# Kernel tuning notes

Measured on AMD Instinct MI355X. Metric: run time of the kernel, lower is better.

## Reference

```python
import jax, jax.numpy as jnp
import numpy as np

T, B, OBS, H, P, L, A = 512, 128, 512, 256, 128, 4, 4


def _ln(x, scale, bias, eps=1e-6):
    mu = jnp.mean(x, axis=-1, keepdims=True)
    var = jnp.mean((x - mu) ** 2, axis=-1, keepdims=True)
    return (x - mu) * jax.lax.rsqrt(var + eps) * scale + bias


def _binop(qi, qj):
    # S5 reset-aware associative operator: elements (A, b, reset_flag)
    Ai, bi, ci = qi
    Aj, bj, cj = qj
    A = (Aj * Ai) * (1.0 - cj) + Aj * cj
    b = (Aj * bi + bj) * (1.0 - cj) + bj * cj
    c = ci * (1.0 - cj) + cj
    return A, b, c


def _s5_layer(x, dones, h0, scale, bias, lam_re, lam_im, b_re, b_im, c_re, c_im, d_vec, log_step, glu_W, glu_b):
    # x: (T,B,H) real, dones: (T,B), h0: (B,P) complex64
    skip = x
    u = _ln(x, scale, bias)                                  # prenorm
    lam = lam_re + 1j * lam_im                               # (P,)
    step = jnp.exp(log_step)                                 # (P,)
    lam_bar = jnp.exp(lam * step)                            # ZOH discretization
    B_bar = ((lam_bar - 1.0) / lam)[:, None] * (b_re + 1j * b_im)  # (P,H)
    Bu = jnp.einsum('tbh,ph->tbp', u.astype(jnp.complex64), B_bar)  # (T,B,P)
    A_el = jnp.concatenate([jnp.ones((1, B, P), jnp.complex64),
                            jnp.broadcast_to(lam_bar.astype(jnp.complex64), (T, B, P))], axis=0)
    b_el = jnp.concatenate([h0[None], Bu], axis=0)
    c_el = jnp.concatenate([jnp.zeros((1, B, 1), jnp.float32), dones[..., None]], axis=0)
    _, xs, _ = jax.lax.associative_scan(_binop, (A_el, b_el, c_el), axis=0)
    xs = xs[1:]                                              # (T,B,P) complex states
    new_h = xs[-1]
    C = c_re + 1j * c_im                                     # (H,P)
    ys = 2.0 * jnp.real(jnp.einsum('tbp,hp->tbh', xs, C)) + d_vec * u  # conj_sym output + D*u
    z = _ln(ys, scale, bias)                                 # gtrxl norm (shared LayerNorm params)
    z = jax.nn.gelu(z)                                       # half_glu1
    z = z * jax.nn.sigmoid(z @ glu_W + glu_b)
    return skip + z, new_h


def setup_inputs() -> dict:
    key = jax.random.key(0)
    ks = jax.random.split(key, 40)
    f32 = jnp.float32

    def n(i, shape, s=1.0):
        return jax.random.normal(ks[i], shape, f32) * s

    inp = {}
    inp['obs'] = n(0, (T, B, OBS))
    inp['dones'] = (jax.random.uniform(ks[1], (T, B)) < 0.01).astype(f32)
    inp['hidden_re'] = jnp.zeros((L, B, P), f32)
    inp['hidden_im'] = jnp.zeros((L, B, P), f32)
    inp['enc0_W'] = n(2, (OBS, 128), 1.0 / np.sqrt(OBS))
    inp['enc0_b'] = jnp.zeros((128,), f32)
    inp['enc1_W'] = n(3, (128, H), 1.0 / np.sqrt(128))
    inp['enc1_b'] = jnp.zeros((H,), f32)
    inp['norm_scale'] = jnp.ones((L, H), f32)
    inp['norm_bias'] = jnp.zeros((L, H), f32)
    inp['Lambda_re'] = -0.5 * jax.random.uniform(ks[4], (L, P), f32) - 0.1
    inp['Lambda_im'] = n(5, (L, P), np.pi)
    inp['B_re'] = n(6, (L, P, H), 1.0 / np.sqrt(H))
    inp['B_im'] = n(7, (L, P, H), 1.0 / np.sqrt(H))
    inp['C_re'] = n(8, (L, H, P), 1.0 / np.sqrt(2 * P))
    inp['C_im'] = n(9, (L, H, P), 1.0 / np.sqrt(2 * P))
    inp['D'] = n(10, (L, H))
    inp['log_step'] = jax.random.uniform(ks[11], (L, P), f32, np.log(1e-3), np.log(1e-1))
    inp['glu_W'] = n(12, (L, H, H), 1.0 / np.sqrt(H))
    inp['glu_b'] = jnp.zeros((L, H), f32)
    inp['ab0_W'] = n(13, (H, 128), 1.0 / np.sqrt(H))
    inp['ab0_b'] = jnp.zeros((128,), f32)
    inp['ab1_W'] = n(14, (128, 128), 1.0 / np.sqrt(128))
    inp['ab1_b'] = jnp.zeros((128,), f32)
    inp['adec_W'] = n(15, (128, A), 0.01 / np.sqrt(128))
    inp['adec_b'] = jnp.full((A,), 0.5, f32)
    inp['log_std'] = jnp.full((A,), -0.7, f32)
    inp['vb0_W'] = n(16, (H, 128), 1.0 / np.sqrt(H))
    inp['vb0_b'] = jnp.zeros((128,), f32)
    inp['vb1_W'] = n(17, (128, 128), 1.0 / np.sqrt(128))
    inp['vb1_b'] = jnp.zeros((128,), f32)
    inp['vdec_W'] = n(18, (128, 1), 1.0 / np.sqrt(128))
    inp['vdec_b'] = jnp.zeros((1,), f32)
    return inp


def reference(obs, dones, hidden_re, hidden_im, enc0_W, enc0_b, enc1_W, enc1_b,
              norm_scale, norm_bias, Lambda_re, Lambda_im, B_re, B_im, C_re, C_im,
              D, log_step, glu_W, glu_b, ab0_W, ab0_b, ab1_W, ab1_b, adec_W, adec_b,
              log_std, vb0_W, vb0_b, vb1_W, vb1_b, vdec_W, vdec_b):
    e = jax.nn.leaky_relu(obs @ enc0_W + enc0_b)
    e = jax.nn.leaky_relu(e @ enc1_W + enc1_b)
    h0 = (hidden_re + 1j * hidden_im).astype(jnp.complex64)  # (L,B,P)
    new_h = []
    for l in range(L):
        e, hl = _s5_layer(e, dones, h0[l], norm_scale[l], norm_bias[l],
                          Lambda_re[l], Lambda_im[l], B_re[l], B_im[l],
                          C_re[l], C_im[l], D[l], log_step[l], glu_W[l], glu_b[l])
        new_h.append(hl)
    new_h = jnp.stack(new_h)
    am = jax.nn.leaky_relu(e @ ab0_W + ab0_b)
    am = jax.nn.leaky_relu(am @ ab1_W + ab1_b)
    am = am @ adec_W + adec_b                                # actor mean (T,B,A)
    v = jax.nn.leaky_relu(e @ vb0_W + vb0_b)
    v = jax.nn.leaky_relu(v @ vb1_W + vb1_b)
    v = v @ vdec_W + vdec_b                                  # critic (T,B,1)
    sc = jnp.broadcast_to(jnp.exp(log_std), am.shape)        # Normal scale (pi params)
    out = jnp.concatenate([am, sc, v], axis=-1)              # (T,B,2A+1)
    return out, jnp.real(new_h), jnp.imag(new_h)
```

## Files before the change

kernel.cpp:

```cpp
#include <hip/hip_runtime.h>
#include <math.h>

#define TT 512
#define BB 128
#define OBSD 512
#define HD 256
#define PD 128
#define LD 4
#define NTB (TT*BB)

typedef __bf16 bf16x8 __attribute__((ext_vector_type(8)));
typedef float  f32x4  __attribute__((ext_vector_type(4)));

__device__ __forceinline__ float bf2f(unsigned short u) {
    return __uint_as_float(((unsigned)u) << 16);
}
__device__ __forceinline__ unsigned short f2bf(float f) {
    unsigned u = __float_as_uint(f);
    unsigned r = (u + 0x7FFFu + ((u >> 16) & 1u)) >> 16;
    return (unsigned short)r;
}
__device__ __forceinline__ float gelu_f(float x) {
    float x3 = x * x * x;
    return 0.5f * x * (1.f + tanhf(0.7978845608028654f * (x + 0.044715f * x3)));
}

__device__ __forceinline__ void stage_tile4(const unsigned short* gbase, int ldk,
                                            int row0, int k0, unsigned short* sm, int tid)
{
    int w = tid >> 6, lane = tid & 63;
#pragma unroll
    for (int p = 0; p < 2; ++p) {
        int r = p * 64 + w * 16 + (lane >> 2);
        const unsigned short* g = gbase + (size_t)(row0 + r) * ldk + k0 + (lane & 3) * 8;
        unsigned short* l = sm + (p * 64 + w * 16) * 32;
        __builtin_amdgcn_global_load_lds(
            (const __attribute__((address_space(1))) void*)g,
            (__attribute__((address_space(3))) void*)l, 16, 0, 0);
    }
}

__device__ __forceinline__ void stage_tile8(const unsigned short* gbase, int ldk,
                                            int row0, int k0, unsigned short* sm, int tid)
{
    int w = tid >> 6, lane = tid & 63;
    int r = w * 16 + (lane >> 2);
    const unsigned short* g = gbase + (size_t)(row0 + r) * ldk + k0 + (lane & 3) * 8;
    unsigned short* l = sm + w * 16 * 32;
    __builtin_amdgcn_global_load_lds(
        (const __attribute__((address_space(1))) void*)g,
        (__attribute__((address_space(3))) void*)l, 16, 0, 0);
}
__device__ __forceinline__ void stage_tile8w(const unsigned short* gbase, int ldk,
                                             int row0, int k0, unsigned short* sm, int tid)
{
    int w = tid >> 6, lane = tid & 63;
#pragma unroll
    for (int p = 0; p < 2; ++p) {
        int r = p * 128 + w * 16 + (lane >> 2);
        const unsigned short* g = gbase + (size_t)(row0 + r) * ldk + k0 + (lane & 3) * 8;
        unsigned short* l = sm + (p * 128 + w * 16) * 32;
        __builtin_amdgcn_global_load_lds(
            (const __attribute__((address_space(1))) void*)g,
            (__attribute__((address_space(3))) void*)l, 16, 0, 0);
    }
}

template<int MODE>
__global__ __launch_bounds__(512) void mgemm2(
    const unsigned short* __restrict__ A, const unsigned short* __restrict__ BT,
    int K, const float* __restrict__ bias,
    const float* __restrict__ lnsc, const float* __restrict__ lnbi,
    const unsigned short* __restrict__ aux1, unsigned short* Xio,
    unsigned short* __restrict__ U, int wU)
{
    __shared__ unsigned short smA[128 * 32];
    __shared__ unsigned short smB[256 * 32];
    __shared__ float2 red[128][4];
    int tid = threadIdx.x;
    int lane = tid & 63, w = tid >> 6;
    int wr = w & 1, wc = w >> 1;
    int m16 = lane & 15, quad = lane >> 4;
    int m0 = blockIdx.x * 128;

    f32x4 acc[4][4] = {};

    for (int k0 = 0; k0 < K; k0 += 32) {
        stage_tile8(A, K, m0, k0, smA, tid);
        stage_tile8w(BT, K, 0, k0, smB, tid);
        __syncthreads();
        bf16x8 af[4], bfr[4];
#pragma unroll
        for (int mi = 0; mi < 4; ++mi)
            af[mi] = *(const bf16x8*)(smA + (wr * 64 + mi * 16 + m16) * 32 + quad * 8);
#pragma unroll
        for (int nj = 0; nj < 4; ++nj)
            bfr[nj] = *(const bf16x8*)(smB + (wc * 64 + nj * 16 + m16) * 32 + quad * 8);
#pragma unroll
        for (int mi = 0; mi < 4; ++mi)
#pragma unroll
            for (int nj = 0; nj < 4; ++nj)
                acc[mi][nj] = __builtin_amdgcn_mfma_f32_16x16x32_bf16(
                    af[mi], bfr[nj], acc[mi][nj], 0, 0, 0);
        __syncthreads();
    }

    int colb = wc * 64 + m16;
    if (MODE == 1) {
#pragma unroll
        for (int mi = 0; mi < 4; ++mi)
#pragma unroll
            for (int nj = 0; nj < 4; ++nj)
#pragma unroll
                for (int r = 0; r < 4; ++r) {
                    int row = m0 + wr * 64 + mi * 16 + quad * 4 + r;
                    U[(size_t)row * 256 + colb + nj * 16] = f2bf(acc[mi][nj][r]);
                }
        return;
    }

    float bn[4];
#pragma unroll
    for (int nj = 0; nj < 4; ++nj) bn[nj] = bias[colb + nj * 16];

#pragma unroll
    for (int mi = 0; mi < 4; ++mi) {
#pragma unroll
        for (int r = 0; r < 4; ++r) {
            int row_l = wr * 64 + mi * 16 + quad * 4 + r;
            size_t rowb = (size_t)(m0 + row_l) * 256;
            float s = 0.f, q = 0.f;
#pragma unroll
            for (int nj = 0; nj < 4; ++nj) {
                size_t idx = rowb + colb + nj * 16;
                float v = acc[mi][nj][r];
                if (MODE == 0) {
                    v += bn[nj]; v = v > 0.f ? v : 0.01f * v;
                    Xio[idx] = f2bf(v);
                } else if (MODE == 2) {
                    v += bn[nj] * bf2f(aux1[idx]);
                } else if (MODE == 3) {
                    float sg = 1.f / (1.f + expf(-(v + bn[nj])));
                    v = bf2f(Xio[idx]) + bf2f(aux1[idx]) * sg;
                    Xio[idx] = f2bf(v);
                }
                acc[mi][nj][r] = v;
                s += v; q += v * v;
            }
            if (MODE != 3 || wU) {
#pragma unroll
                for (int mask = 1; mask < 16; mask <<= 1) {
                    s += __shfl_xor(s, mask);
                    q += __shfl_xor(q, mask);
                }
                if (m16 == 0) red[row_l][wc] = float2{s, q};
            }
        }
    }
    if (MODE == 3 && !wU) return;
    __syncthreads();

    float ls[4], lb[4];
#pragma unroll
    for (int nj = 0; nj < 4; ++nj) { ls[nj] = lnsc[colb + nj * 16]; lb[nj] = lnbi[colb + nj * 16]; }
#pragma unroll
    for (int mi = 0; mi < 4; ++mi) {
#pragma unroll
        for (int r = 0; r < 4; ++r) {
            int row_l = wr * 64 + mi * 16 + quad * 4 + r;
            float2 t0 = red[row_l][0], t1 = red[row_l][1], t2 = red[row_l][2], t3 = red[row_l][3];
            float S = t0.x + t1.x + t2.x + t3.x;
            float Q = t0.y + t1.y + t2.y + t3.y;
            float mu = S * (1.f / 256.f);
            float var = Q * (1.f / 256.f) - mu * mu;
            float rstd = rsqrtf(var + 1e-6f);
            size_t rowb = (size_t)(m0 + row_l) * 256;
#pragma unroll
            for (int nj = 0; nj < 4; ++nj) {
                float o = (acc[mi][nj][r] - mu) * rstd * ls[nj] + lb[nj];
                if (MODE == 2) o = gelu_f(o);
                U[rowb + colb + nj * 16] = f2bf(o);
            }
        }
    }
}

__global__ __launch_bounds__(256) void mgemm(
    const unsigned short* __restrict__ A, const unsigned short* __restrict__ BT,
    unsigned short* __restrict__ C, int M, int N, int K,
    const float* __restrict__ bias)
{
    __shared__ unsigned short smA[128 * 32];
    __shared__ unsigned short smB[128 * 32];
    int tid = threadIdx.x;
    int lane = tid & 63, w = tid >> 6;
    int wr = w & 1, wc = w >> 1;
    int m16 = lane & 15, quad = lane >> 4;
    int m0 = blockIdx.x * 128, n0 = blockIdx.y * 128;

    f32x4 acc[4][4] = {};
    for (int k0 = 0; k0 < K; k0 += 32) {
        stage_tile4(A, K, m0, k0, smA, tid);
        stage_tile4(BT, K, n0, k0, smB, tid);
        __syncthreads();
        bf16x8 af[4], bfr[4];
#pragma unroll
        for (int mi = 0; mi < 4; ++mi)
            af[mi] = *(const bf16x8*)(smA + (wr * 64 + mi * 16 + m16) * 32 + quad * 8);
#pragma unroll
        for (int nj = 0; nj < 4; ++nj)
            bfr[nj] = *(const bf16x8*)(smB + (wc * 64 + nj * 16 + m16) * 32 + quad * 8);
#pragma unroll
        for (int mi = 0; mi < 4; ++mi)
#pragma unroll
            for (int nj = 0; nj < 4; ++nj)
                acc[mi][nj] = __builtin_amdgcn_mfma_f32_16x16x32_bf16(
                    af[mi], bfr[nj], acc[mi][nj], 0, 0, 0);
        __syncthreads();
    }
#pragma unroll
    for (int mi = 0; mi < 4; ++mi)
#pragma unroll
        for (int nj = 0; nj < 4; ++nj) {
            int mg = m0 + wr * 64 + mi * 16 + quad * 4;
            int ng = n0 + wc * 64 + nj * 16 + m16;
            float bv = bias[ng];
#pragma unroll
            for (int r = 0; r < 4; ++r) {
                float v = acc[mi][nj][r] + bv;
                v = v > 0.f ? v : 0.01f * v;
                C[(size_t)(mg + r) * N + ng] = f2bf(v);
            }
        }
}

__global__ __launch_bounds__(512) void scan2_k(
    const unsigned short* __restrict__ bu, unsigned short* __restrict__ xs,
    const float* __restrict__ dones,
    const float* __restrict__ h0re, const float* __restrict__ h0im,
    const float* __restrict__ lamre, const float* __restrict__ lamim,
    const float* __restrict__ lstep,
    float* __restrict__ outre, float* __restrict__ outim)
{
    __shared__ float sdone[TT];
    __shared__ float4 ssum[8][64];
    __shared__ float2 shin[8][64];
    int tid = threadIdx.x;
    int b  = blockIdx.x >> 1;
    int ph = blockIdx.x & 1;
    int chunk = tid >> 6, pl = tid & 63;
    int p = ph * 64 + pl;
    sdone[tid] = dones[tid * BB + b];
    float lr = lamre[p], li = lamim[p];
    float st = expf(lstep[p]);
    float er = expf(lr * st);
    float ar = er * cosf(li * st);
    float ai = er * sinf(li * st);
    __syncthreads();

    int t0 = chunk * 64;
    unsigned buf[64];
    float Ar = 1.f, Ai = 0.f, br = 0.f, bi = 0.f;
#pragma unroll
    for (int j = 0; j < 64; ++j) {
        size_t base = ((size_t)(t0 + j) * BB + b) * 256;
        unsigned short rr = bu[base + p];
        unsigned short ii = bu[base + 128 + p];
        buf[j] = ((unsigned)ii << 16) | rr;
        float bur = bf2f(rr), bui = bf2f(ii);
        if (sdone[t0 + j] != 0.f) {
            Ar = 0.f; Ai = 0.f; br = bur; bi = bui;
        } else {
            float nAr = ar * Ar - ai * Ai;
            float nAi = ar * Ai + ai * Ar;
            float nbr = fmaf(ar, br, fmaf(-ai, bi, bur));
            float nbi = fmaf(ar, bi, fmaf(ai, br, bui));
            Ar = nAr; Ai = nAi; br = nbr; bi = nbi;
        }
    }
    ssum[chunk][pl] = float4{Ar, Ai, br, bi};
    __syncthreads();
    if (tid < 64) {
        int gid = b * 128 + p;
        float hr = h0re[gid], hi = h0im[gid];
#pragma unroll
        for (int c = 0; c < 8; ++c) {
            shin[c][pl] = float2{hr, hi};
            float4 s = ssum[c][pl];
            float nhr = fmaf(s.x, hr, fmaf(-s.y, hi, s.z));
            float nhi = fmaf(s.x, hi, fmaf(s.y, hr, s.w));
            hr = nhr; hi = nhi;
        }
        outre[gid] = hr; outim[gid] = hi;
    }
    __syncthreads();
    float hr = shin[chunk][pl].x, hi = shin[chunk][pl].y;
#pragma unroll
    for (int j = 0; j < 64; ++j) {
        unsigned v = buf[j];
        float bur = bf2f((unsigned short)(v & 0xFFFFu));
        float bui = bf2f((unsigned short)(v >> 16));
        float nr, ni;
        if (sdone[t0 + j] != 0.f) { nr = bur; ni = bui; }
        else {
            nr = fmaf(ar, hr, fmaf(-ai, hi, bur));
            ni = fmaf(ar, hi, fmaf(ai, hr, bui));
        }
        hr = nr; hi = ni;
        size_t base = ((size_t)(t0 + j) * BB + b) * 256;
        xs[base + p] = f2bf(nr);
        xs[base + 128 + p] = f2bf(ni);
    }
}

__global__ __launch_bounds__(256) void prep_k(
    const float* __restrict__ Br, const float* __restrict__ Bi,
    const float* __restrict__ Cr, const float* __restrict__ Ci,
    const float* __restrict__ Lr, const float* __restrict__ Li,
    const float* __restrict__ ls, unsigned short* bbarT, unsigned short* ccatT)
{
    int gid = blockIdx.x * 256 + threadIdx.x;
    int l = gid >> 15;
    int rem = gid & 32767;
    int p = rem >> 8;
    int h = rem & 255;
    float lr = Lr[l * PD + p], li = Li[l * PD + p];
    float st = expf(ls[l * PD + p]);
    float er = expf(lr * st);
    float lbr = er * cosf(li * st);
    float lbi = er * sinf(li * st);
    float nr = lbr - 1.f, ni = lbi;
    float den = lr * lr + li * li;
    float fr = (nr * lr + ni * li) / den;
    float fi = (ni * lr - nr * li) / den;
    float bre = Br[(size_t)(l * PD + p) * HD + h];
    float bim = Bi[(size_t)(l * PD + p) * HD + h];
    size_t lb = (size_t)l * 65536;
    bbarT[lb + (size_t)p * 256 + h]         = f2bf(fr * bre - fi * bim);
    bbarT[lb + (size_t)(128 + p) * 256 + h] = f2bf(fr * bim + fi * bre);
    float cre = Cr[(size_t)(l * HD + h) * PD + p];
    float cim = Ci[(size_t)(l * HD + h) * PD + p];
    ccatT[lb + (size_t)h * 256 + p]         = f2bf(2.f * cre);
    ccatT[lb + (size_t)h * 256 + 128 + p]   = f2bf(-2.f * cim);
}

__global__ __launch_bounds__(256) void tcvt_k(const float* __restrict__ in,
    unsigned short* __restrict__ out, int K, int N)
{
    int gid = blockIdx.x * 256 + threadIdx.x;
    if (gid >= K * N) return;
    int k = gid / N, n = gid - k * N;
    out[(size_t)n * K + k] = f2bf(in[gid]);
}

__global__ __launch_bounds__(256) void cvt_k(const float* __restrict__ in,
    unsigned short* __restrict__ out)
{
    size_t gid = (size_t)blockIdx.x * 256 + threadIdx.x;
    float4 v = ((const float4*)in)[gid];
    ushort4 o = { f2bf(v.x), f2bf(v.y), f2bf(v.z), f2bf(v.w) };
    ((ushort4*)out)[gid] = o;
}

__global__ __launch_bounds__(256) void head_k(
    const unsigned short* __restrict__ am2, const unsigned short* __restrict__ v2,
    const float* __restrict__ adW, const float* __restrict__ adb,
    const float* __restrict__ lstd,
    const float* __restrict__ vdW, const float* __restrict__ vdb,
    float* out)
{
    int wid = threadIdx.x >> 6, lane = threadIdx.x & 63;
    size_t row = (size_t)blockIdx.x * 4 + wid;
    float a1 = bf2f(am2[row * 128 + lane]);
    float a2 = bf2f(am2[row * 128 + 64 + lane]);
    float w1 = bf2f(v2[row * 128 + lane]);
    float w2 = bf2f(v2[row * 128 + 64 + lane]);
    float vals[5];
#pragma unroll
    for (int a = 0; a < 4; ++a)
        vals[a] = a1 * adW[lane * 4 + a] + a2 * adW[(lane + 64) * 4 + a];
    vals[4] = w1 * vdW[lane] + w2 * vdW[64 + lane];
#pragma unroll
    for (int off = 32; off; off >>= 1)
#pragma unroll
        for (int k = 0; k < 5; ++k) vals[k] += __shfl_xor(vals[k], off);
    if (lane == 0) {
        size_t o = row * 9;
#pragma unroll
        for (int a = 0; a < 4; ++a) out[o + a] = vals[a] + adb[a];
#pragma unroll
        for (int a = 0; a < 4; ++a) out[o + 4 + a] = expf(lstd[a]);
        out[o + 8] = vals[4] + vdb[0];
    }
}

extern "C" void kernel_launch(void* const* d_in, const int* in_sizes, int n_in,
                              void* d_out, int out_size, void* d_ws, size_t ws_size,
                              hipStream_t stream) {
    (void)in_sizes; (void)n_in; (void)out_size; (void)ws_size;
    const float* obs     = (const float*)d_in[0];
    const float* dones   = (const float*)d_in[1];
    const float* hre     = (const float*)d_in[2];
    const float* him     = (const float*)d_in[3];
    const float* enc0_W  = (const float*)d_in[4];
    const float* enc0_b  = (const float*)d_in[5];
    const float* enc1_W  = (const float*)d_in[6];
    const float* enc1_b  = (const float*)d_in[7];
    const float* nsc     = (const float*)d_in[8];
    const float* nbi     = (const float*)d_in[9];
    const float* Lre     = (const float*)d_in[10];
    const float* Lim     = (const float*)d_in[11];
    const float* B_re    = (const float*)d_in[12];
    const float* B_im    = (const float*)d_in[13];
    const float* C_re    = (const float*)d_in[14];
    const float* C_im    = (const float*)d_in[15];
    const float* Dv      = (const float*)d_in[16];
    const float* lstep   = (const float*)d_in[17];
    const float* glu_W   = (const float*)d_in[18];
    const float* glu_b   = (const float*)d_in[19];
    const float* ab0_W   = (const float*)d_in[20];
    const float* ab0_b   = (const float*)d_in[21];
    const float* ab1_W   = (const float*)d_in[22];
    const float* ab1_b   = (const float*)d_in[23];
    const float* adec_W  = (const float*)d_in[24];
    const float* adec_b  = (const float*)d_in[25];
    const float* log_std = (const float*)d_in[26];
    const float* vb0_W   = (const float*)d_in[27];
    const float* vb0_b   = (const float*)d_in[28];
    const float* vb1_W   = (const float*)d_in[29];
    const float* vb1_b   = (const float*)d_in[30];
    const float* vdec_W  = (const float*)d_in[31];
    const float* vdec_b  = (const float*)d_in[32];

    const size_t MB = (size_t)1 << 20;
    char* wsb = (char*)d_ws;
    unsigned short* OBSBF = (unsigned short*)(wsb);
    unsigned short* XS    = (unsigned short*)(wsb);
    unsigned short* AM1   = (unsigned short*)(wsb);
    unsigned short* V1    = (unsigned short*)(wsb + 16 * MB);
    unsigned short* AM2   = (unsigned short*)(wsb + 32 * MB);
    unsigned short* V2    = (unsigned short*)(wsb + 48 * MB);
    unsigned short* U1    = (unsigned short*)(wsb + 64 * MB);
    unsigned short* X     = (unsigned short*)(wsb + 96 * MB);
    unsigned short* U     = (unsigned short*)(wsb + 128 * MB);
    unsigned short* BU    = (unsigned short*)(wsb + 160 * MB);
    char* wgt = wsb + 192 * MB;
    unsigned short* BBART = (unsigned short*)(wgt);
    unsigned short* CCATT = (unsigned short*)(wgt + 512 * 1024);
    unsigned short* GLUT  = (unsigned short*)(wgt + 1024 * 1024);
    unsigned short* E0T   = (unsigned short*)(wgt + 1536 * 1024);
    unsigned short* E1T   = (unsigned short*)(wgt + 1664 * 1024);
    unsigned short* AB0T  = (unsigned short*)(wgt + 1728 * 1024);
    unsigned short* AB1T  = (unsigned short*)(wgt + 1792 * 1024);
    unsigned short* VB0T  = (unsigned short*)(wgt + 1824 * 1024);
    unsigned short* VB1T  = (unsigned short*)(wgt + 1888 * 1024);

    float* out   = (float*)d_out;
    float* outre = out + (size_t)NTB * 9;
    float* outim = outre + LD * BB * PD;

    prep_k<<<512, 256, 0, stream>>>(B_re, B_im, C_re, C_im, Lre, Lim, lstep, BBART, CCATT);
    tcvt_k<<<256, 256, 0, stream>>>(enc0_W, E0T, 512, 128);
    tcvt_k<<<128, 256, 0, stream>>>(enc1_W, E1T, 128, 256);
    for (int l = 0; l < LD; ++l)
        tcvt_k<<<256, 256, 0, stream>>>(glu_W + (size_t)l * 65536, GLUT + (size_t)l * 65536, 256, 256);
    tcvt_k<<<128, 256, 0, stream>>>(ab0_W, AB0T, 256, 128);
    tcvt_k<<<64, 256, 0, stream>>>(ab1_W, AB1T, 128, 128);
    tcvt_k<<<128, 256, 0, stream>>>(vb0_W, VB0T, 256, 128);
    tcvt_k<<<64, 256, 0, stream>>>(vb1_W, VB1T, 128, 128);
    cvt_k<<<32768, 256, 0, stream>>>(obs, OBSBF);

    mgemm<<<dim3(512, 1), 256, 0, stream>>>(OBSBF, E0T, U1, NTB, 128, 512, enc0_b);
    mgemm2<0><<<512, 512, 0, stream>>>(U1, E1T, 128, enc1_b, nsc, nbi, nullptr, X, U, 1);

    for (int l = 0; l < LD; ++l) {
        mgemm2<1><<<512, 512, 0, stream>>>(U, BBART + (size_t)l * 65536, 256,
                                           nullptr, nullptr, nullptr, nullptr, nullptr, BU, 0);
        scan2_k<<<256, 512, 0, stream>>>(BU, XS, dones, hre + l * BB * PD, him + l * BB * PD,
                                         Lre + l * PD, Lim + l * PD, lstep + l * PD,
                                         outre + l * BB * PD, outim + l * BB * PD);
        mgemm2<2><<<512, 512, 0, stream>>>(XS, CCATT + (size_t)l * 65536, 256,
                                           Dv + l * HD, nsc + l * HD, nbi + l * HD, U, nullptr, U, 1);
        const float* nsc2 = nsc + ((l + 1 < LD) ? (l + 1) * HD : 0);
        const float* nbi2 = nbi + ((l + 1 < LD) ? (l + 1) * HD : 0);
        mgemm2<3><<<512, 512, 0, stream>>>(U, GLUT + (size_t)l * 65536, 256,
                                           glu_b + l * HD, nsc2, nbi2, U, X, U, (l + 1 < LD) ? 1 : 0);
    }

    mgemm<<<dim3(512, 1), 256, 0, stream>>>(X, AB0T, AM1, NTB, 128, 256, ab0_b);
    mgemm<<<dim3(512, 1), 256, 0, stream>>>(AM1, AB1T, AM2, NTB, 128, 128, ab1_b);
    mgemm<<<dim3(512, 1), 256, 0, stream>>>(X, VB0T, V1, NTB, 128, 256, vb0_b);
    mgemm<<<dim3(512, 1), 256, 0, stream>>>(V1, VB1T, V2, NTB, 128, 128, vb1_b);
    head_k<<<NTB / 4, 256, 0, stream>>>(AM2, V2, adec_W, adec_b, log_std, vdec_W, vdec_b, out);
}
```

Measured before the change: 1.004 ms.

## Fuse obs bf16 conversion into encoder GEMM and interleave complex layout

Removes the separate fp32-to-bf16 conversion pass over the observation tensor by converting inside a new encoder GEMM kernel that reads fp32 directly, so the bf16 copy is never written to or read back from memory. It also changes the complex state layout from split real/imag halves to interleaved pairs, so the scan does one 32-bit load and one 32-bit store per element instead of two 16-bit accesses. The B-bar and C weight layouts are permuted to match, keeping the GEMM contractions the same. The fused GEMM reloads fp32 A tiles without double buffering, which may stall its main loop.

Result: slower. 1.199 ms (+19.5%).

```diff
diff --git a/kernel.cpp b/kernel.cpp
--- a/kernel.cpp
+++ b/kernel.cpp
@@ -234,6 +234,62 @@
         }
 }
 
+__global__ __launch_bounds__(256) void mgemm_obs(
+    const float* __restrict__ A, const unsigned short* __restrict__ BT,
+    unsigned short* __restrict__ C, int M, int N, int K,
+    const float* __restrict__ bias)
+{
+    __shared__ unsigned short smA[128 * 32];
+    __shared__ unsigned short smB[128 * 32];
+    int tid = threadIdx.x;
+    int lane = tid & 63, w = tid >> 6;
+    int wr = w & 1, wc = w >> 1;
+    int m16 = lane & 15, quad = lane >> 4;
+    int m0 = blockIdx.x * 128, n0 = blockIdx.y * 128;
+
+    f32x4 acc[4][4] = {};
+    for (int k0 = 0; k0 < K; k0 += 32) {
+#pragma unroll
+        for (int it = 0; it < 4; ++it) {
+            int idx = it * 256 + tid;
+            int r = idx >> 3, kq = (idx & 7) * 4;
+            float4 v = *(const float4*)(A + (size_t)(m0 + r) * K + k0 + kq);
+            ushort4 o = { f2bf(v.x), f2bf(v.y), f2bf(v.z), f2bf(v.w) };
+            *(ushort4*)(smA + r * 32 + kq) = o;
+        }
+        stage_tile4(BT, K, n0, k0, smB, tid);
+        __syncthreads();
+        bf16x8 af[4], bfr[4];
+#pragma unroll
+        for (int mi = 0; mi < 4; ++mi)
+            af[mi] = *(const bf16x8*)(smA + (wr * 64 + mi * 16 + m16) * 32 + quad * 8);
+#pragma unroll
+        for (int nj = 0; nj < 4; ++nj)
+            bfr[nj] = *(const bf16x8*)(smB + (wc * 64 + nj * 16 + m16) * 32 + quad * 8);
+#pragma unroll
+        for (int mi = 0; mi < 4; ++mi)
+#pragma unroll
+            for (int nj = 0; nj < 4; ++nj)
+                acc[mi][nj] = __builtin_amdgcn_mfma_f32_16x16x32_bf16(
+                    af[mi], bfr[nj], acc[mi][nj], 0, 0, 0);
+        __syncthreads();
+    }
+#pragma unroll
+    for (int mi = 0; mi < 4; ++mi)
+#pragma unroll
+        for (int nj = 0; nj < 4; ++nj) {
+            int mg = m0 + wr * 64 + mi * 16 + quad * 4;
+            int ng = n0 + wc * 64 + nj * 16 + m16;
+            float bv = bias[ng];
+#pragma unroll
+            for (int r = 0; r < 4; ++r) {
+                float v = acc[mi][nj][r] + bv;
+                v = v > 0.f ? v : 0.01f * v;
+                C[(size_t)(mg + r) * N + ng] = f2bf(v);
+            }
+        }
+}
+
 __global__ __launch_bounds__(512) void scan2_k(
     const unsigned short* __restrict__ bu, unsigned short* __restrict__ xs,
     const float* __restrict__ dones,
@@ -263,11 +319,11 @@
     float Ar = 1.f, Ai = 0.f, br = 0.f, bi = 0.f;
 #pragma unroll
     for (int j = 0; j < 64; ++j) {
-        size_t base = ((size_t)(t0 + j) * BB + b) * 256;
-        unsigned short rr = bu[base + p];
-        unsigned short ii = bu[base + 128 + p];
-        buf[j] = ((unsigned)ii << 16) | rr;
-        float bur = bf2f(rr), bui = bf2f(ii);
+        size_t off = ((size_t)(t0 + j) * BB + b) * 256 + 2 * p;
+        unsigned v = *(const unsigned*)(bu + off);
+        buf[j] = v;
+        float bur = bf2f((unsigned short)(v & 0xFFFFu));
+        float bui = bf2f((unsigned short)(v >> 16));
         if (sdone[t0 + j] != 0.f) {
             Ar = 0.f; Ai = 0.f; br = bur; bi = bui;
         } else {
@@ -307,9 +363,8 @@
             ni = fmaf(ar, hi, fmaf(ai, hr, bui));
         }
         hr = nr; hi = ni;
-        size_t base = ((size_t)(t0 + j) * BB + b) * 256;
-        xs[base + p] = f2bf(nr);
-        xs[base + 128 + p] = f2bf(ni);
+        size_t off = ((size_t)(t0 + j) * BB + b) * 256 + 2 * p;
+        *(unsigned*)(xs + off) = ((unsigned)f2bf(ni) << 16) | f2bf(nr);
     }
 }
 
@@ -336,12 +391,12 @@
     float bre = Br[(size_t)(l * PD + p) * HD + h];
     float bim = Bi[(size_t)(l * PD + p) * HD + h];
     size_t lb = (size_t)l * 65536;
-    bbarT[lb + (size_t)p * 256 + h]         = f2bf(fr * bre - fi * bim);
-    bbarT[lb + (size_t)(128 + p) * 256 + h] = f2bf(fr * bim + fi * bre);
+    bbarT[lb + (size_t)(2 * p) * 256 + h]     = f2bf(fr * bre - fi * bim);
+    bbarT[lb + (size_t)(2 * p + 1) * 256 + h] = f2bf(fr * bim + fi * bre);
     float cre = Cr[(size_t)(l * HD + h) * PD + p];
     float cim = Ci[(size_t)(l * HD + h) * PD + p];
-    ccatT[lb + (size_t)h * 256 + p]         = f2bf(2.f * cre);
-    ccatT[lb + (size_t)h * 256 + 128 + p]   = f2bf(-2.f * cim);
+    ccatT[lb + (size_t)h * 256 + 2 * p]     = f2bf(2.f * cre);
+    ccatT[lb + (size_t)h * 256 + 2 * p + 1] = f2bf(-2.f * cim);
 }
 
 __global__ __launch_bounds__(256) void tcvt_k(const float* __restrict__ in,
@@ -351,15 +406,6 @@
     if (gid >= K * N) return;
     int k = gid / N, n = gid - k * N;
     out[(size_t)n * K + k] = f2bf(in[gid]);
-}
-
-__global__ __launch_bounds__(256) void cvt_k(const float* __restrict__ in,
-    unsigned short* __restrict__ out)
-{
-    size_t gid = (size_t)blockIdx.x * 256 + threadIdx.x;
-    float4 v = ((const float4*)in)[gid];
-    ushort4 o = { f2bf(v.x), f2bf(v.y), f2bf(v.z), f2bf(v.w) };
-    ((ushort4*)out)[gid] = o;
 }
 
 __global__ __launch_bounds__(256) void head_k(
@@ -434,7 +480,6 @@
 
     const size_t MB = (size_t)1 << 20;
     char* wsb = (char*)d_ws;
-    unsigned short* OBSBF = (unsigned short*)(wsb);
     unsigned short* XS    = (unsigned short*)(wsb);
     unsigned short* AM1   = (unsigned short*)(wsb);
     unsigned short* V1    = (unsigned short*)(wsb + 16 * MB);
@@ -468,9 +513,8 @@
     tcvt_k<<<64, 256, 0, stream>>>(ab1_W, AB1T, 128, 128);
     tcvt_k<<<128, 256, 0, stream>>>(vb0_W, VB0T, 256, 128);
     tcvt_k<<<64, 256, 0, stream>>>(vb1_W, VB1T, 128, 128);
-    cvt_k<<<32768, 256, 0, stream>>>(obs, OBSBF);
-
-    mgemm<<<dim3(512, 1), 256, 0, stream>>>(OBSBF, E0T, U1, NTB, 128, 512, enc0_b);
+
+    mgemm_obs<<<dim3(512, 1), 256, 0, stream>>>(obs, E0T, U1, NTB, 128, 512, enc0_b);
     mgemm2<0><<<512, 512, 0, stream>>>(U1, E1T, 128, enc1_b, nsc, nbi, nullptr, X, U, 1);
 
     for (int l = 0; l < LD; ++l) {
```

## Restructure GEMMs to 64-row tiles with transposed MFMA, fuse obs conversion, interleave complex layout

Applied to the files above, without the earlier changes.

All GEMMs now use 64-row tiles with 256-thread blocks and swap the MFMA operands, so each lane holds four consecutive columns and can write or read them as one ushort4. The obs fp32-to-bf16 conversion is folded into the first encoder GEMM's staging, which removes a separate pass over the input. Real and imaginary parts in the Bbar/C weights and in the BU/XS buffers are interleaved so the scan does single 32-bit loads and stores. The trade-off is smaller tiles, which give less operand reuse per block, and register-path staging for obs instead of direct-to-LDS loads.

Measured after the change: 984.7 us. About the same (-1.9%).

```diff
diff --git a/kernel.cpp b/kernel.cpp
--- a/kernel.cpp
+++ b/kernel.cpp
@@ -25,213 +25,218 @@
     return 0.5f * x * (1.f + tanhf(0.7978845608028654f * (x + 0.044715f * x3)));
 }
 
-__device__ __forceinline__ void stage_tile4(const unsigned short* gbase, int ldk,
-                                            int row0, int k0, unsigned short* sm, int tid)
-{
-    int w = tid >> 6, lane = tid & 63;
-#pragma unroll
-    for (int p = 0; p < 2; ++p) {
-        int r = p * 64 + w * 16 + (lane >> 2);
-        const unsigned short* g = gbase + (size_t)(row0 + r) * ldk + k0 + (lane & 3) * 8;
-        unsigned short* l = sm + (p * 64 + w * 16) * 32;
-        __builtin_amdgcn_global_load_lds(
-            (const __attribute__((address_space(1))) void*)g,
-            (__attribute__((address_space(3))) void*)l, 16, 0, 0);
-    }
-}
-
-__device__ __forceinline__ void stage_tile8(const unsigned short* gbase, int ldk,
-                                            int row0, int k0, unsigned short* sm, int tid)
-{
-    int w = tid >> 6, lane = tid & 63;
-    int r = w * 16 + (lane >> 2);
-    const unsigned short* g = gbase + (size_t)(row0 + r) * ldk + k0 + (lane & 3) * 8;
-    unsigned short* l = sm + w * 16 * 32;
-    __builtin_amdgcn_global_load_lds(
-        (const __attribute__((address_space(1))) void*)g,
-        (__attribute__((address_space(3))) void*)l, 16, 0, 0);
-}
-__device__ __forceinline__ void stage_tile8w(const unsigned short* gbase, int ldk,
-                                             int row0, int k0, unsigned short* sm, int tid)
-{
-    int w = tid >> 6, lane = tid & 63;
-#pragma unroll
-    for (int p = 0; p < 2; ++p) {
-        int r = p * 128 + w * 16 + (lane >> 2);
-        const unsigned short* g = gbase + (size_t)(row0 + r) * ldk + k0 + (lane & 3) * 8;
-        unsigned short* l = sm + (p * 128 + w * 16) * 32;
-        __builtin_amdgcn_global_load_lds(
-            (const __attribute__((address_space(1))) void*)g,
-            (__attribute__((address_space(3))) void*)l, 16, 0, 0);
-    }
-}
-
-template<int MODE>
-__global__ __launch_bounds__(512) void mgemm2(
+template<int MODE, int NJ>
+__global__ __launch_bounds__(256) void mgemm2(
     const unsigned short* __restrict__ A, const unsigned short* __restrict__ BT,
     int K, const float* __restrict__ bias,
     const float* __restrict__ lnsc, const float* __restrict__ lnbi,
     const unsigned short* __restrict__ aux1, unsigned short* Xio,
     unsigned short* __restrict__ U, int wU)
 {
-    __shared__ unsigned short smA[128 * 32];
-    __shared__ unsigned short smB[256 * 32];
-    __shared__ float2 red[128][4];
+    const int N = NJ * 64;
+    __shared__ unsigned short smA[64 * 32];
+    __shared__ unsigned short smB[NJ * 64 * 32];
+    __shared__ float2 red[64][4];
     int tid = threadIdx.x;
     int lane = tid & 63, w = tid >> 6;
-    int wr = w & 1, wc = w >> 1;
     int m16 = lane & 15, quad = lane >> 4;
-    int m0 = blockIdx.x * 128;
-
-    f32x4 acc[4][4] = {};
+    int m0 = blockIdx.x * 64;
+
+    f32x4 acc[4][NJ] = {};
 
     for (int k0 = 0; k0 < K; k0 += 32) {
-        stage_tile8(A, K, m0, k0, smA, tid);
-        stage_tile8w(BT, K, 0, k0, smB, tid);
+        {
+            const unsigned short* g = A + (size_t)(m0 + (tid >> 2)) * K + k0 + (tid & 3) * 8;
+            unsigned short* l = smA + tid * 8;
+            __builtin_amdgcn_global_load_lds(
+                (const __attribute__((address_space(1))) void*)g,
+                (__attribute__((address_space(3))) void*)l, 16, 0, 0);
+        }
+#pragma unroll
+        for (int p = 0; p < NJ; ++p) {
+            const unsigned short* g = BT + (size_t)(p * 64 + (tid >> 2)) * K + k0 + (tid & 3) * 8;
+            unsigned short* l = smB + p * 2048 + tid * 8;
+            __builtin_amdgcn_global_load_lds(
+                (const __attribute__((address_space(1))) void*)g,
+                (__attribute__((address_space(3))) void*)l, 16, 0, 0);
+        }
         __syncthreads();
-        bf16x8 af[4], bfr[4];
+        bf16x8 af[4], bfr[NJ];
 #pragma unroll
         for (int mi = 0; mi < 4; ++mi)
-            af[mi] = *(const bf16x8*)(smA + (wr * 64 + mi * 16 + m16) * 32 + quad * 8);
-#pragma unroll
-        for (int nj = 0; nj < 4; ++nj)
-            bfr[nj] = *(const bf16x8*)(smB + (wc * 64 + nj * 16 + m16) * 32 + quad * 8);
+            af[mi] = *(const bf16x8*)(smA + (mi * 16 + m16) * 32 + quad * 8);
+#pragma unroll
+        for (int nj = 0; nj < NJ; ++nj)
+            bfr[nj] = *(const bf16x8*)(smB + (w * NJ * 16 + nj * 16 + m16) * 32 + quad * 8);
 #pragma unroll
         for (int mi = 0; mi < 4; ++mi)
 #pragma unroll
-            for (int nj = 0; nj < 4; ++nj)
+            for (int nj = 0; nj < NJ; ++nj)
                 acc[mi][nj] = __builtin_amdgcn_mfma_f32_16x16x32_bf16(
-                    af[mi], bfr[nj], acc[mi][nj], 0, 0, 0);
+                    bfr[nj], af[mi], acc[mi][nj], 0, 0, 0);
         __syncthreads();
     }
 
-    int colb = wc * 64 + m16;
+    int colb = w * NJ * 16 + quad * 4;
+
     if (MODE == 1) {
 #pragma unroll
-        for (int mi = 0; mi < 4; ++mi)
-#pragma unroll
-            for (int nj = 0; nj < 4; ++nj)
-#pragma unroll
-                for (int r = 0; r < 4; ++r) {
-                    int row = m0 + wr * 64 + mi * 16 + quad * 4 + r;
-                    U[(size_t)row * 256 + colb + nj * 16] = f2bf(acc[mi][nj][r]);
+        for (int mi = 0; mi < 4; ++mi) {
+            size_t rowb = (size_t)(m0 + mi * 16 + m16) * N;
+#pragma unroll
+            for (int nj = 0; nj < NJ; ++nj) {
+                ushort4 o = { f2bf(acc[mi][nj][0]), f2bf(acc[mi][nj][1]),
+                              f2bf(acc[mi][nj][2]), f2bf(acc[mi][nj][3]) };
+                *(ushort4*)(U + rowb + colb + nj * 16) = o;
+            }
+        }
+        return;
+    }
+
+    float4 bn[NJ];
+#pragma unroll
+    for (int nj = 0; nj < NJ; ++nj) bn[nj] = *(const float4*)(bias + colb + nj * 16);
+
+#pragma unroll
+    for (int mi = 0; mi < 4; ++mi) {
+        size_t rowb = (size_t)(m0 + mi * 16 + m16) * N;
+        float s = 0.f, q = 0.f;
+#pragma unroll
+        for (int nj = 0; nj < NJ; ++nj) {
+            ushort4 a1, xo;
+            if (MODE == 2 || MODE == 3) a1 = *(const ushort4*)(aux1 + rowb + colb + nj * 16);
+            if (MODE == 3)              xo = *(const ushort4*)(Xio + rowb + colb + nj * 16);
+            float vv[4];
+#pragma unroll
+            for (int r = 0; r < 4; ++r) {
+                float v = acc[mi][nj][r];
+                float bv = (r == 0) ? bn[nj].x : (r == 1) ? bn[nj].y : (r == 2) ? bn[nj].z : bn[nj].w;
+                if (MODE == 0 || MODE == 4) {
+                    v += bv; v = v > 0.f ? v : 0.01f * v;
+                } else if (MODE == 2) {
+                    float u = bf2f(r == 0 ? a1.x : r == 1 ? a1.y : r == 2 ? a1.z : a1.w);
+                    v += bv * u;
+                } else if (MODE == 3) {
+                    float zz = bf2f(r == 0 ? a1.x : r == 1 ? a1.y : r == 2 ? a1.z : a1.w);
+                    float xx = bf2f(r == 0 ? xo.x : r == 1 ? xo.y : r == 2 ? xo.z : xo.w);
+                    float sg = 1.f / (1.f + expf(-(v + bv)));
+                    v = xx + zz * sg;
                 }
-        return;
-    }
-
-    float bn[4];
-#pragma unroll
-    for (int nj = 0; nj < 4; ++nj) bn[nj] = bias[colb + nj * 16];
-
-#pragma unroll
-    for (int mi = 0; mi < 4; ++mi) {
-#pragma unroll
-        for (int r = 0; r < 4; ++r) {
-            int row_l = wr * 64 + mi * 16 + quad * 4 + r;
-            size_t rowb = (size_t)(m0 + row_l) * 256;
-            float s = 0.f, q = 0.f;
-#pragma unroll
-            for (int nj = 0; nj < 4; ++nj) {
-                size_t idx = rowb + colb + nj * 16;
-                float v = acc[mi][nj][r];
-                if (MODE == 0) {
-                    v += bn[nj]; v = v > 0.f ? v : 0.01f * v;
-                    Xio[idx] = f2bf(v);
-                } else if (MODE == 2) {
-                    v += bn[nj] * bf2f(aux1[idx]);
-                } else if (MODE == 3) {
-                    float sg = 1.f / (1.f + expf(-(v + bn[nj])));
-                    v = bf2f(Xio[idx]) + bf2f(aux1[idx]) * sg;
-                    Xio[idx] = f2bf(v);
-                }
+                vv[r] = v;
                 acc[mi][nj][r] = v;
                 s += v; q += v * v;
             }
-            if (MODE != 3 || wU) {
-#pragma unroll
-                for (int mask = 1; mask < 16; mask <<= 1) {
-                    s += __shfl_xor(s, mask);
-                    q += __shfl_xor(q, mask);
-                }
-                if (m16 == 0) red[row_l][wc] = float2{s, q};
+            if (MODE == 0 || MODE == 3) {
+                ushort4 o = { f2bf(vv[0]), f2bf(vv[1]), f2bf(vv[2]), f2bf(vv[3]) };
+                *(ushort4*)(Xio + rowb + colb + nj * 16) = o;
+            } else if (MODE == 4) {
+                ushort4 o = { f2bf(vv[0]), f2bf(vv[1]), f2bf(vv[2]), f2bf(vv[3]) };
+                *(ushort4*)(U + rowb + colb + nj * 16) = o;
             }
         }
-    }
-    if (MODE == 3 && !wU) return;
+        if (MODE != 4 && (MODE != 3 || wU)) {
+            s += __shfl_xor(s, 16); q += __shfl_xor(q, 16);
+            s += __shfl_xor(s, 32); q += __shfl_xor(q, 32);
+            if (quad == 0) red[mi * 16 + m16][w] = float2{s, q};
+        }
+    }
+    if (MODE == 4 || (MODE == 3 && !wU)) return;
     __syncthreads();
 
-    float ls[4], lb[4];
-#pragma unroll
-    for (int nj = 0; nj < 4; ++nj) { ls[nj] = lnsc[colb + nj * 16]; lb[nj] = lnbi[colb + nj * 16]; }
+    float4 ls[NJ], lb[NJ];
+#pragma unroll
+    for (int nj = 0; nj < NJ; ++nj) {
+        ls[nj] = *(const float4*)(lnsc + colb + nj * 16);
+        lb[nj] = *(const float4*)(lnbi + colb + nj * 16);
+    }
 #pragma unroll
     for (int mi = 0; mi < 4; ++mi) {
-#pragma unroll
-        for (int r = 0; r < 4; ++r) {
-            int row_l = wr * 64 + mi * 16 + quad * 4 + r;
-            float2 t0 = red[row_l][0], t1 = red[row_l][1], t2 = red[row_l][2], t3 = red[row_l][3];
-            float S = t0.x + t1.x + t2.x + t3.x;
-            float Q = t0.y + t1.y + t2.y + t3.y;
-            float mu = S * (1.f / 256.f);
-            float var = Q * (1.f / 256.f) - mu * mu;
-            float rstd = rsqrtf(var + 1e-6f);
-            size_t rowb = (size_t)(m0 + row_l) * 256;
-#pragma unroll
-            for (int nj = 0; nj < 4; ++nj) {
-                float o = (acc[mi][nj][r] - mu) * rstd * ls[nj] + lb[nj];
-                if (MODE == 2) o = gelu_f(o);
-                U[rowb + colb + nj * 16] = f2bf(o);
+        int row_l = mi * 16 + m16;
+        float2 t0 = red[row_l][0], t1 = red[row_l][1], t2 = red[row_l][2], t3 = red[row_l][3];
+        float S = t0.x + t1.x + t2.x + t3.x;
+        float Q = t0.y + t1.y + t2.y + t3.y;
+        float mu = S * (1.f / 256.f);
+        float var = Q * (1.f / 256.f) - mu * mu;
+        float rstd = rsqrtf(var + 1e-6f);
+        size_t rowb = (size_t)(m0 + row_l) * N;
+#pragma unroll
+        for (int nj = 0; nj < NJ; ++nj) {
+            float o[4];
+#pragma unroll
+            for (int r = 0; r < 4; ++r) {
+                float sc = (r == 0) ? ls[nj].x : (r == 1) ? ls[nj].y : (r == 2) ? ls[nj].z : ls[nj].w;
+                float bi = (r == 0) ? lb[nj].x : (r == 1) ? lb[nj].y : (r == 2) ? lb[nj].z : lb[nj].w;
+                float v = (acc[mi][nj][r] - mu) * rstd * sc + bi;
+                if (MODE == 2) v = gelu_f(v);
+                o[r] = v;
             }
-        }
-    }
-}
-
-__global__ __launch_bounds__(256) void mgemm(
-    const unsigned short* __restrict__ A, const unsigned short* __restrict__ BT,
-    unsigned short* __restrict__ C, int M, int N, int K,
-    const float* __restrict__ bias)
-{
-    __shared__ unsigned short smA[128 * 32];
-    __shared__ unsigned short smB[128 * 32];
+            ushort4 ov = { f2bf(o[0]), f2bf(o[1]), f2bf(o[2]), f2bf(o[3]) };
+            *(ushort4*)(U + rowb + colb + nj * 16) = ov;
+        }
+    }
+}
+
+__global__ __launch_bounds__(256) void mgemm_obs(
+    const float* __restrict__ A, const unsigned short* __restrict__ BT,
+    unsigned short* __restrict__ U, const float* __restrict__ bias)
+{
+    const int K = 512, NJ = 2, N = 128;
+    __shared__ unsigned short smA[64 * 32];
+    __shared__ unsigned short smB[NJ * 64 * 32];
     int tid = threadIdx.x;
     int lane = tid & 63, w = tid >> 6;
-    int wr = w & 1, wc = w >> 1;
     int m16 = lane & 15, quad = lane >> 4;
-    int m0 = blockIdx.x * 128, n0 = blockIdx.y * 128;
-
-    f32x4 acc[4][4] = {};
+    int m0 = blockIdx.x * 64;
+
+    f32x4 acc[4][NJ] = {};
     for (int k0 = 0; k0 < K; k0 += 32) {
-        stage_tile4(A, K, m0, k0, smA, tid);
-        stage_tile4(BT, K, n0, k0, smB, tid);
+#pragma unroll
+        for (int p = 0; p < 2; ++p) {
+            int idx = p * 256 + tid;
+            int r = idx >> 3, kq = (idx & 7) * 4;
+            float4 v = *(const float4*)(A + (size_t)(m0 + r) * K + k0 + kq);
+            ushort4 o = { f2bf(v.x), f2bf(v.y), f2bf(v.z), f2bf(v.w) };
+            *(ushort4*)(smA + r * 32 + kq) = o;
+        }
+#pragma unroll
+        for (int p = 0; p < NJ; ++p) {
+            const unsigned short* g = BT + (size_t)(p * 64 + (tid >> 2)) * K + k0 + (tid & 3) * 8;
+            unsigned short* l = smB + p * 2048 + tid * 8;
+            __builtin_amdgcn_global_load_lds(
+                (const __attribute__((address_space(1))) void*)g,
+                (__attribute__((address_space(3))) void*)l, 16, 0, 0);
+        }
         __syncthreads();
-        bf16x8 af[4], bfr[4];
+        bf16x8 af[4], bfr[NJ];
 #pragma unroll
         for (int mi = 0; mi < 4; ++mi)
-            af[mi] = *(const bf16x8*)(smA + (wr * 64 + mi * 16 + m16) * 32 + quad * 8);
-#pragma unroll
-        for (int nj = 0; nj < 4; ++nj)
-            bfr[nj] = *(const bf16x8*)(smB + (wc * 64 + nj * 16 + m16) * 32 + quad * 8);
+            af[mi] = *(const bf16x8*)(smA + (mi * 16 + m16) * 32 + quad * 8);
+#pragma unroll
+        for (int nj = 0; nj < NJ; ++nj)
+            bfr[nj] = *(const bf16x8*)(smB + (w * NJ * 16 + nj * 16 + m16) * 32 + quad * 8);
 #pragma unroll
         for (int mi = 0; mi < 4; ++mi)
 #pragma unroll
-            for (int nj = 0; nj < 4; ++nj)
+            for (int nj = 0; nj < NJ; ++nj)
                 acc[mi][nj] = __builtin_amdgcn_mfma_f32_16x16x32_bf16(
-                    af[mi], bfr[nj], acc[mi][nj], 0, 0, 0);
+                    bfr[nj], af[mi], acc[mi][nj], 0, 0, 0);
         __syncthreads();
     }
-#pragma unroll
-    for (int mi = 0; mi < 4; ++mi)
-#pragma unroll
-        for (int nj = 0; nj < 4; ++nj) {
-            int mg = m0 + wr * 64 + mi * 16 + quad * 4;
-            int ng = n0 + wc * 64 + nj * 16 + m16;
-            float bv = bias[ng];
-#pragma unroll
-            for (int r = 0; r < 4; ++r) {
-                float v = acc[mi][nj][r] + bv;
-                v = v > 0.f ? v : 0.01f * v;
-                C[(size_t)(mg + r) * N + ng] = f2bf(v);
-            }
-        }
+    int colb = w * NJ * 16 + quad * 4;
+#pragma unroll
+    for (int mi = 0; mi < 4; ++mi) {
+        size_t rowb = (size_t)(m0 + mi * 16 + m16) * N;
+#pragma unroll
+        for (int nj = 0; nj < NJ; ++nj) {
+            float4 bv = *(const float4*)(bias + colb + nj * 16);
+            float v0 = acc[mi][nj][0] + bv.x; v0 = v0 > 0.f ? v0 : 0.01f * v0;
+            float v1 = acc[mi][nj][1] + bv.y; v1 = v1 > 0.f ? v1 : 0.01f * v1;
+            float v2 = acc[mi][nj][2] + bv.z; v2 = v2 > 0.f ? v2 : 0.01f * v2;
+            float v3 = acc[mi][nj][3] + bv.w; v3 = v3 > 0.f ? v3 : 0.01f * v3;
+            ushort4 o = { f2bf(v0), f2bf(v1), f2bf(v2), f2bf(v3) };
+            *(ushort4*)(U + rowb + colb + nj * 16) = o;
+        }
+    }
 }
 
 __global__ __launch_bounds__(512) void scan2_k(
@@ -263,11 +268,11 @@
     float Ar = 1.f, Ai = 0.f, br = 0.f, bi = 0.f;
 #pragma unroll
     for (int j = 0; j < 64; ++j) {
-        size_t base = ((size_t)(t0 + j) * BB + b) * 256;
-        unsigned short rr = bu[base + p];
-        unsigned short ii = bu[base + 128 + p];
-        buf[j] = ((unsigned)ii << 16) | rr;
-        float bur = bf2f(rr), bui = bf2f(ii);
+        size_t off = ((size_t)(t0 + j) * BB + b) * 256 + 2 * p;
+        unsigned v = *(const unsigned*)(bu + off);
+        buf[j] = v;
+        float bur = bf2f((unsigned short)(v & 0xFFFFu));
+        float bui = bf2f((unsigned short)(v >> 16));
         if (sdone[t0 + j] != 0.f) {
             Ar = 0.f; Ai = 0.f; br = bur; bi = bui;
         } else {
@@ -307,9 +312,8 @@
             ni = fmaf(ar, hi, fmaf(ai, hr, bui));
         }
         hr = nr; hi = ni;
-        size_t base = ((size_t)(t0 + j) * BB + b) * 256;
-        xs[base + p] = f2bf(nr);
-        xs[base + 128 + p] = f2bf(ni);
+        size_t off = ((size_t)(t0 + j) * BB + b) * 256 + 2 * p;
+        *(unsigned*)(xs + off) = ((unsigned)f2bf(ni) << 16) | f2bf(nr);
     }
 }
 
@@ -336,12 +340,12 @@
     float bre = Br[(size_t)(l * PD + p) * HD + h];
     float bim = Bi[(size_t)(l * PD + p) * HD + h];
     size_t lb = (size_t)l * 65536;
-    bbarT[lb + (size_t)p * 256 + h]         = f2bf(fr * bre - fi * bim);
-    bbarT[lb + (size_t)(128 + p) * 256 + h] = f2bf(fr * bim + fi * bre);
+    bbarT[lb + (size_t)(2 * p) * 256 + h]     = f2bf(fr * bre - fi * bim);
+    bbarT[lb + (size_t)(2 * p + 1) * 256 + h] = f2bf(fr * bim + fi * bre);
     float cre = Cr[(size_t)(l * HD + h) * PD + p];
     float cim = Ci[(size_t)(l * HD + h) * PD + p];
-    ccatT[lb + (size_t)h * 256 + p]         = f2bf(2.f * cre);
-    ccatT[lb + (size_t)h * 256 + 128 + p]   = f2bf(-2.f * cim);
+    ccatT[lb + (size_t)h * 256 + 2 * p]     = f2bf(2.f * cre);
+    ccatT[lb + (size_t)h * 256 + 2 * p + 1] = f2bf(-2.f * cim);
 }
 
 __global__ __launch_bounds__(256) void tcvt_k(const float* __restrict__ in,
@@ -351,15 +355,6 @@
     if (gid >= K * N) return;
     int k = gid / N, n = gid - k * N;
     out[(size_t)n * K + k] = f2bf(in[gid]);
-}
-
-__global__ __launch_bounds__(256) void cvt_k(const float* __restrict__ in,
-    unsigned short* __restrict__ out)
-{
-    size_t gid = (size_t)blockIdx.x * 256 + threadIdx.x;
-    float4 v = ((const float4*)in)[gid];
-    ushort4 o = { f2bf(v.x), f2bf(v.y), f2bf(v.z), f2bf(v.w) };
-    ((ushort4*)out)[gid] = o;
 }
 
 __global__ __launch_bounds__(256) void head_k(
@@ -434,7 +429,6 @@
 
     const size_t MB = (size_t)1 << 20;
     char* wsb = (char*)d_ws;
-    unsigned short* OBSBF = (unsigned short*)(wsb);
     unsigned short* XS    = (unsigned short*)(wsb);
     unsigned short* AM1   = (unsigned short*)(wsb);
     unsigned short* V1    = (unsigned short*)(wsb + 16 * MB);
@@ -468,28 +462,27 @@
     tcvt_k<<<64, 256, 0, stream>>>(ab1_W, AB1T, 128, 128);
     tcvt_k<<<128, 256, 0, stream>>>(vb0_W, VB0T, 256, 128);
     tcvt_k<<<64, 256, 0, stream>>>(vb1_W, VB1T, 128, 128);
-    cvt_k<<<32768, 256, 0, stream>>>(obs, OBSBF);
-
-    mgemm<<<dim3(512, 1), 256, 0, stream>>>(OBSBF, E0T, U1, NTB, 128, 512, enc0_b);
-    mgemm2<0><<<512, 512, 0, stream>>>(U1, E1T, 128, enc1_b, nsc, nbi, nullptr, X, U, 1);
+
+    mgemm_obs<<<1024, 256, 0, stream>>>(obs, E0T, U1, enc0_b);
+    mgemm2<0, 4><<<1024, 256, 0, stream>>>(U1, E1T, 128, enc1_b, nsc, nbi, nullptr, X, U, 1);
 
     for (int l = 0; l < LD; ++l) {
-        mgemm2<1><<<512, 512, 0, stream>>>(U, BBART + (size_t)l * 65536, 256,
-                                           nullptr, nullptr, nullptr, nullptr, nullptr, BU, 0);
+        mgemm2<1, 4><<<1024, 256, 0, stream>>>(U, BBART + (size_t)l * 65536, 256,
+                                               nullptr, nullptr, nullptr, nullptr, nullptr, BU, 0);
         scan2_k<<<256, 512, 0, stream>>>(BU, XS, dones, hre + l * BB * PD, him + l * BB * PD,
                                          Lre + l * PD, Lim + l * PD, lstep + l * PD,
                                          outre + l * BB * PD, outim + l * BB * PD);
-        mgemm2<2><<<512, 512, 0, stream>>>(XS, CCATT + (size_t)l * 65536, 256,
-                                           Dv + l * HD, nsc + l * HD, nbi + l * HD, U, nullptr, U, 1);
+        mgemm2<2, 4><<<1024, 256, 0, stream>>>(XS, CCATT + (size_t)l * 65536, 256,
+                                               Dv + l * HD, nsc + l * HD, nbi + l * HD, U, nullptr, U, 1);
         const float* nsc2 = nsc + ((l + 1 < LD) ? (l + 1) * HD : 0);
         const float* nbi2 = nbi + ((l + 1 < LD) ? (l + 1) * HD : 0);
-        mgemm2<3><<<512, 512, 0, stream>>>(U, GLUT + (size_t)l * 65536, 256,
-                                           glu_b + l * HD, nsc2, nbi2, U, X, U, (l + 1 < LD) ? 1 : 0);
-    }
-
-    mgemm<<<dim3(512, 1), 256, 0, stream>>>(X, AB0T, AM1, NTB, 128, 256, ab0_b);
-    mgemm<<<dim3(512, 1), 256, 0, stream>>>(AM1, AB1T, AM2, NTB, 128, 128, ab1_b);
-    mgemm<<<dim3(512, 1), 256, 0, stream>>>(X, VB0T, V1, NTB, 128, 256, vb0_b);
-    mgemm<<<dim3(512, 1), 256, 0, stream>>>(V1, VB1T, V2, NTB, 128, 128, vb1_b);
+        mgemm2<3, 4><<<1024, 256, 0, stream>>>(U, GLUT + (size_t)l * 65536, 256,
+                                               glu_b + l * HD, nsc2, nbi2, U, X, U, (l + 1 < LD) ? 1 : 0);
+    }
+
+    mgemm2<4, 2><<<1024, 256, 0, stream>>>(X, AB0T, 256, ab0_b, nullptr, nullptr, nullptr, nullptr, AM1, 0);
+    mgemm2<4, 2><<<1024, 256, 0, stream>>>(AM1, AB1T, 128, ab1_b, nullptr, nullptr, nullptr, nullptr, AM2, 0);
+    mgemm2<4, 2><<<1024, 256, 0, stream>>>(X, VB0T, 256, vb0_b, nullptr, nullptr, nullptr, nullptr, V1, 0);
+    mgemm2<4, 2><<<1024, 256, 0, stream>>>(V1, VB1T, 128, vb1_b, nullptr, nullptr, nullptr, nullptr, V2, 0);
     head_k<<<NTB / 4, 256, 0, stream>>>(AM2, V2, adec_W, adec_b, log_std, vdec_W, vdec_b, out);
 }
```
